# Optimization experiments

Measured on AMD Instinct MI355X. Metric: run time of the kernel, lower is better.

## Reference

```python
import jax, jax.numpy as jnp
import numpy as np

B, N, C = 32, 4096, 768
H = 12
HD = C // H
SCALE = HD ** -0.5


def setup_inputs() -> dict:
    key = jax.random.key(0)
    ks = jax.random.split(key, 5)
    x = jax.random.normal(ks[0], (B, N, C), dtype=jnp.float32)
    s = 1.0 / np.sqrt(C)
    Wq = jax.random.normal(ks[1], (C, C), dtype=jnp.float32) * s
    Wk = jax.random.normal(ks[2], (C, C), dtype=jnp.float32) * s
    Wv = jax.random.normal(ks[3], (C, C), dtype=jnp.float32) * s
    Wp = jax.random.normal(ks[4], (C, C), dtype=jnp.float32) * s
    bp = jnp.zeros((C,), dtype=jnp.float32)
    return {"x": x, "Wq": Wq, "Wk": Wk, "Wv": Wv, "Wp": Wp, "bp": bp}


def reference(x, Wq, Wk, Wv, Wp, bp):
    # single-query (CLS token) cross-attention over N keys
    q = (x[:, 0, :] @ Wq).reshape(B, H, HD)            # [B,H,hd]
    k = (x @ Wk).reshape(B, N, H, HD)                  # [B,N,H,hd]
    v = (x @ Wv).reshape(B, N, H, HD)                  # [B,N,H,hd]
    attn = jnp.einsum('bhd,bnhd->bhn', q, k) * SCALE   # [B,H,N]
    attn = jax.nn.softmax(attn, axis=-1)
    o = jnp.einsum('bhn,bnhd->bhd', attn, v)           # [B,H,hd]
    o = o.reshape(B, 1, C)
    out = o @ Wp + bp                                  # [B,1,C]
    return out
```

## Files before the change

### kernel.cpp

```cpp
#include <hip/hip_runtime.h>
#include <hip/hip_bf16.h>

#define B 32
#define N 4096
#define C 768
#define H 12
#define HD 64

__global__ __launch_bounds__(256) void k1_q(const float* __restrict__ x,
                                            const float* __restrict__ Wq,
                                            float* __restrict__ q) {
    __shared__ float xs[C];
    int b = blockIdx.x / 3;
    int coBase = (blockIdx.x % 3) * 256;
    int t = threadIdx.x;
    for (int i = t; i < C; i += 256) xs[i] = x[(size_t)b * N * C + i];
    __syncthreads();
    int co = coBase + t;
    float acc = 0.f;
    for (int c = 0; c < C; ++c) acc = fmaf(xs[c], Wq[(size_t)c * C + co], acc);
    q[b * C + co] = acc;
}

__global__ __launch_bounds__(256) void k2_qk(const float* __restrict__ q,
                                             const float* __restrict__ Wk,
                                             float* __restrict__ qk,
                                             float* __restrict__ xa) {
    int id = blockIdx.x * 256 + threadIdx.x;
    xa[id] = 0.f;
    int b = id / (H * C);
    int r = id % (H * C);
    int h = r / C;
    int c = r % C;
    const float* wrow = Wk + (size_t)c * C + h * HD;
    const float* qrow = q + b * C + h * HD;
    float acc = 0.f;
#pragma unroll
    for (int j = 0; j < HD / 4; ++j) {
        float4 wv = *(const float4*)(wrow + j * 4);
        float4 qv = *(const float4*)(qrow + j * 4);
        acc += wv.x * qv.x + wv.y * qv.y + wv.z * qv.z + wv.w * qv.w;
    }
    qk[id] = acc * 0.125f;
}

__global__ __launch_bounds__(256) void k3_scores(const float* __restrict__ x,
                                                 const float* __restrict__ qk,
                                                 float* __restrict__ p) {
    __shared__ float4 qks[H * C / 4];
    int b = blockIdx.x >> 5;
    int chunk = blockIdx.x & 31;
    int t = threadIdx.x;
    const float4* qg = (const float4*)(qk + (size_t)b * H * C);
    for (int i = t; i < H * C / 4; i += 256) qks[i] = qg[i];
    __syncthreads();
    int wave = t >> 6, lane = t & 63;
    for (int rr = 0; rr < 32; ++rr) {
        int n = chunk * 128 + wave * 32 + rr;
        const float4* xr = (const float4*)(x + ((size_t)b * N + n) * C);
        float4 X0 = xr[lane];
        float4 X1 = xr[64 + lane];
        float4 X2 = xr[128 + lane];
        float partial[H];
#pragma unroll
        for (int h = 0; h < H; ++h) {
            float4 a0 = qks[h * 192 + lane];
            float4 a1 = qks[h * 192 + 64 + lane];
            float4 a2 = qks[h * 192 + 128 + lane];
            float s = X0.x * a0.x;
            s = fmaf(X0.y, a0.y, s); s = fmaf(X0.z, a0.z, s); s = fmaf(X0.w, a0.w, s);
            s = fmaf(X1.x, a1.x, s); s = fmaf(X1.y, a1.y, s);
            s = fmaf(X1.z, a1.z, s); s = fmaf(X1.w, a1.w, s);
            s = fmaf(X2.x, a2.x, s); s = fmaf(X2.y, a2.y, s);
            s = fmaf(X2.z, a2.z, s); s = fmaf(X2.w, a2.w, s);
            partial[h] = s;
        }
#pragma unroll
        for (int h = 0; h < H; ++h) {
            float v = partial[h];
            for (int off = 32; off > 0; off >>= 1) v += __shfl_xor(v, off);
            partial[h] = v;
        }
        float ov = 0.f;
#pragma unroll
        for (int h = 0; h < H; ++h)
            if (lane == h) ov = partial[h];
        if (lane < H) p[((size_t)b * N + n) * H + lane] = ov;
    }
}

__global__ __launch_bounds__(256) void k4_softmax(float* __restrict__ p) {
    int b = blockIdx.x / H, h = blockIdx.x % H;
    float* pr = p + (size_t)b * N * H + h;
    int t = threadIdx.x;
    float vals[16];
    float m = -1e30f;
#pragma unroll
    for (int i = 0; i < 16; ++i) {
        vals[i] = pr[(size_t)(t + i * 256) * H];
        m = fmaxf(m, vals[i]);
    }
    __shared__ float red[4];
    __shared__ float red2[4];
    for (int off = 32; off > 0; off >>= 1) m = fmaxf(m, __shfl_xor(m, off));
    if ((t & 63) == 0) red[t >> 6] = m;
    __syncthreads();
    m = fmaxf(fmaxf(red[0], red[1]), fmaxf(red[2], red[3]));
    float s = 0.f;
#pragma unroll
    for (int i = 0; i < 16; ++i) {
        vals[i] = __expf(vals[i] - m);
        s += vals[i];
    }
    for (int off = 32; off > 0; off >>= 1) s += __shfl_xor(s, off);
    if ((t & 63) == 0) red2[t >> 6] = s;
    __syncthreads();
    s = red2[0] + red2[1] + red2[2] + red2[3];
    float inv = 1.f / s;
#pragma unroll
    for (int i = 0; i < 16; ++i) pr[(size_t)(t + i * 256) * H] = vals[i] * inv;
}

__global__ __launch_bounds__(256) void k5_xa(const float* __restrict__ x,
                                             const float* __restrict__ p,
                                             float* __restrict__ xa) {
    int gid = blockIdx.x;
    int b = gid / 24;
    int rem = gid % 24;
    int cc = rem / 4;
    int ns = rem % 4;
    int t = threadIdx.x;
    int g = t >> 6;
    int c = cc * 128 + (t & 63) * 2;
    float2 a0 = {0.f, 0.f}, a1 = {0.f, 0.f}, a2 = {0.f, 0.f};
    int n0 = ns * 1024;
    for (int n = n0; n < n0 + 1024; ++n) {
        const float2 xv = *(const float2*)(x + ((size_t)b * N + n) * C + c);
        const float* pr = p + ((size_t)b * N + n) * H + g * 3;
        float p0 = pr[0], p1 = pr[1], p2 = pr[2];
        a0.x = fmaf(p0, xv.x, a0.x); a0.y = fmaf(p0, xv.y, a0.y);
        a1.x = fmaf(p1, xv.x, a1.x); a1.y = fmaf(p1, xv.y, a1.y);
        a2.x = fmaf(p2, xv.x, a2.x); a2.y = fmaf(p2, xv.y, a2.y);
    }
    int h0 = g * 3;
    atomicAdd(&xa[((size_t)b * H + h0    ) * C + c    ], a0.x);
    atomicAdd(&xa[((size_t)b * H + h0    ) * C + c + 1], a0.y);
    atomicAdd(&xa[((size_t)b * H + h0 + 1) * C + c    ], a1.x);
    atomicAdd(&xa[((size_t)b * H + h0 + 1) * C + c + 1], a1.y);
    atomicAdd(&xa[((size_t)b * H + h0 + 2) * C + c    ], a2.x);
    atomicAdd(&xa[((size_t)b * H + h0 + 2) * C + c + 1], a2.y);
}

__global__ __launch_bounds__(256) void k6_o(const float* __restrict__ xa,
                                            const float* __restrict__ Wv,
                                            float* __restrict__ o) {
    int id = blockIdx.x * 256 + threadIdx.x;
    int b = id / C;
    int r = id % C;
    int h = r / HD;
    const float* xr = xa + ((size_t)b * H + h) * C;
    const float* wcol = Wv + r;
    float acc = 0.f;
    for (int c = 0; c < C; ++c) acc = fmaf(xr[c], wcol[(size_t)c * C], acc);
    o[id] = acc;
}

__global__ __launch_bounds__(256) void k7_out(const float* __restrict__ o,
                                              const float* __restrict__ Wp,
                                              const float* __restrict__ bp,
                                              float* __restrict__ out) {
    int id = blockIdx.x * 256 + threadIdx.x;
    int b = id / C;
    int co = id % C;
    const float* orow = o + (size_t)b * C;
    float acc = bp[co];
    for (int c = 0; c < C; ++c) acc = fmaf(orow[c], Wp[(size_t)c * C + co], acc);
    out[id] = acc;
}

extern "C" void kernel_launch(void* const* d_in, const int* in_sizes, int n_in,
                              void* d_out, int out_size, void* d_ws, size_t ws_size,
                              hipStream_t stream) {
    const float* x  = (const float*)d_in[0];
    const float* Wq = (const float*)d_in[1];
    const float* Wk = (const float*)d_in[2];
    const float* Wv = (const float*)d_in[3];
    const float* Wp = (const float*)d_in[4];
    const float* bp = (const float*)d_in[5];
    float* out = (float*)d_out;

    float* ws = (float*)d_ws;
    float* q  = ws;
    float* qk = q + B * C;
    float* p  = qk + (size_t)B * H * C;
    float* xa = p + (size_t)B * N * H;
    float* o  = xa + (size_t)B * H * C;

    k1_q      <<<96,   256, 0, stream>>>(x, Wq, q);
    k2_qk     <<<1152, 256, 0, stream>>>(q, Wk, qk, xa);
    k3_scores <<<1024, 256, 0, stream>>>(x, qk, p);
    k4_softmax<<<384,  256, 0, stream>>>(p);
    k5_xa     <<<768,  256, 0, stream>>>(x, p, xa);
    k6_o      <<<96,   256, 0, stream>>>(xa, Wv, o);
    k7_out    <<<96,   256, 0, stream>>>(o, Wp, bp, out);
}
```

Before: 985.8 us.

## Transpose scores layout, transpose Wk, and restructure score and weighted-sum kernels

Adds a transpose kernel so k2 reads Wk transposed with coalesced row access, and changes the score buffer to [B,H,N] so softmax reads contiguous float4 rows. k3 now uses 512-thread blocks that process two rows at a time with register prefetch of the next rows. k5 is reorganized to stage probabilities in shared memory and keep 12 head accumulators per thread, with a rolling prefetch of x. The aim is to cut strided memory access and the repeated reads of x in the weighted-sum pass. The cost is an extra transpose kernel, more workspace, and higher register pressure in k3 and k5.

```diff
diff --git a/kernel.cpp b/kernel.cpp
--- a/kernel.cpp
+++ b/kernel.cpp
@@ -6,6 +6,19 @@
 #define C 768
 #define H 12
 #define HD 64
+
+__global__ __launch_bounds__(256) void kT(const float* __restrict__ A, float* __restrict__ AT) {
+    __shared__ float tile[32][33];
+    int bx = blockIdx.x % 24, by = blockIdx.x / 24;
+    int tx = threadIdx.x & 31, ty = threadIdx.x >> 5;
+#pragma unroll
+    for (int i = 0; i < 32; i += 8)
+        tile[ty + i][tx] = A[(size_t)(by * 32 + ty + i) * C + bx * 32 + tx];
+    __syncthreads();
+#pragma unroll
+    for (int i = 0; i < 32; i += 8)
+        AT[(size_t)(bx * 32 + ty + i) * C + by * 32 + tx] = tile[tx][ty + i];
+}
 
 __global__ __launch_bounds__(256) void k1_q(const float* __restrict__ x,
                                             const float* __restrict__ Wq,
@@ -23,132 +36,176 @@
 }
 
 __global__ __launch_bounds__(256) void k2_qk(const float* __restrict__ q,
-                                             const float* __restrict__ Wk,
+                                             const float* __restrict__ WkT,
                                              float* __restrict__ qk,
                                              float* __restrict__ xa) {
-    int id = blockIdx.x * 256 + threadIdx.x;
-    xa[id] = 0.f;
-    int b = id / (H * C);
-    int r = id % (H * C);
-    int h = r / C;
-    int c = r % C;
-    const float* wrow = Wk + (size_t)c * C + h * HD;
-    const float* qrow = q + b * C + h * HD;
-    float acc = 0.f;
-#pragma unroll
-    for (int j = 0; j < HD / 4; ++j) {
-        float4 wv = *(const float4*)(wrow + j * 4);
-        float4 qv = *(const float4*)(qrow + j * 4);
-        acc += wv.x * qv.x + wv.y * qv.y + wv.z * qv.z + wv.w * qv.w;
-    }
-    qk[id] = acc * 0.125f;
-}
-
-__global__ __launch_bounds__(256) void k3_scores(const float* __restrict__ x,
+    int b = blockIdx.x / H, h = blockIdx.x % H;
+    int t = threadIdx.x;
+    __shared__ float qs[HD];
+    if (t < HD) qs[t] = q[b * C + h * HD + t];
+    float* xab = xa + ((size_t)b * H + h) * C;
+    xab[t] = 0.f; xab[t + 256] = 0.f; xab[t + 512] = 0.f;
+    __syncthreads();
+    float a0 = 0.f, a1 = 0.f, a2 = 0.f;
+    const float* wbase = WkT + (size_t)h * HD * C;
+    for (int d = 0; d < HD; ++d) {
+        float qd = qs[d];
+        const float* wr = wbase + (size_t)d * C;
+        a0 = fmaf(qd, wr[t], a0);
+        a1 = fmaf(qd, wr[t + 256], a1);
+        a2 = fmaf(qd, wr[t + 512], a2);
+    }
+    float* qkb = qk + ((size_t)b * H + h) * C;
+    qkb[t] = a0 * 0.125f; qkb[t + 256] = a1 * 0.125f; qkb[t + 512] = a2 * 0.125f;
+}
+
+__global__ __launch_bounds__(512) void k3_scores(const float* __restrict__ x,
                                                  const float* __restrict__ qk,
-                                                 float* __restrict__ p) {
-    __shared__ float4 qks[H * C / 4];
+                                                 float* __restrict__ p2) {
+    __shared__ float4 qks[H * 192];
     int b = blockIdx.x >> 5;
     int chunk = blockIdx.x & 31;
     int t = threadIdx.x;
     const float4* qg = (const float4*)(qk + (size_t)b * H * C);
-    for (int i = t; i < H * C / 4; i += 256) qks[i] = qg[i];
+    for (int i = t; i < H * 192; i += 512) qks[i] = qg[i];
     __syncthreads();
     int wave = t >> 6, lane = t & 63;
-    for (int rr = 0; rr < 32; ++rr) {
-        int n = chunk * 128 + wave * 32 + rr;
-        const float4* xr = (const float4*)(x + ((size_t)b * N + n) * C);
-        float4 X0 = xr[lane];
-        float4 X1 = xr[64 + lane];
-        float4 X2 = xr[128 + lane];
-        float partial[H];
+    int n0 = chunk * 128 + wave * 16;
+    const float4* xbase = (const float4*)(x + (size_t)b * N * C);
+    float4 Xc[2][3], Xn[2][3];
+#pragma unroll
+    for (int r = 0; r < 2; ++r)
+#pragma unroll
+        for (int j = 0; j < 3; ++j)
+            Xc[r][j] = xbase[(size_t)(n0 + r) * 192 + j * 64 + lane];
+    for (int pr = 0; pr < 8; ++pr) {
+        int n = n0 + pr * 2;
+        if (pr < 7) {
+#pragma unroll
+            for (int r = 0; r < 2; ++r)
+#pragma unroll
+                for (int j = 0; j < 3; ++j)
+                    Xn[r][j] = xbase[(size_t)(n + 2 + r) * 192 + j * 64 + lane];
+        }
+        float s0[H], s1[H];
 #pragma unroll
         for (int h = 0; h < H; ++h) {
             float4 a0 = qks[h * 192 + lane];
             float4 a1 = qks[h * 192 + 64 + lane];
             float4 a2 = qks[h * 192 + 128 + lane];
-            float s = X0.x * a0.x;
-            s = fmaf(X0.y, a0.y, s); s = fmaf(X0.z, a0.z, s); s = fmaf(X0.w, a0.w, s);
-            s = fmaf(X1.x, a1.x, s); s = fmaf(X1.y, a1.y, s);
-            s = fmaf(X1.z, a1.z, s); s = fmaf(X1.w, a1.w, s);
-            s = fmaf(X2.x, a2.x, s); s = fmaf(X2.y, a2.y, s);
-            s = fmaf(X2.z, a2.z, s); s = fmaf(X2.w, a2.w, s);
-            partial[h] = s;
+            float u = Xc[0][0].x * a0.x;
+            u = fmaf(Xc[0][0].y, a0.y, u); u = fmaf(Xc[0][0].z, a0.z, u); u = fmaf(Xc[0][0].w, a0.w, u);
+            u = fmaf(Xc[0][1].x, a1.x, u); u = fmaf(Xc[0][1].y, a1.y, u);
+            u = fmaf(Xc[0][1].z, a1.z, u); u = fmaf(Xc[0][1].w, a1.w, u);
+            u = fmaf(Xc[0][2].x, a2.x, u); u = fmaf(Xc[0][2].y, a2.y, u);
+            u = fmaf(Xc[0][2].z, a2.z, u); u = fmaf(Xc[0][2].w, a2.w, u);
+            s0[h] = u;
+            float v = Xc[1][0].x * a0.x;
+            v = fmaf(Xc[1][0].y, a0.y, v); v = fmaf(Xc[1][0].z, a0.z, v); v = fmaf(Xc[1][0].w, a0.w, v);
+            v = fmaf(Xc[1][1].x, a1.x, v); v = fmaf(Xc[1][1].y, a1.y, v);
+            v = fmaf(Xc[1][1].z, a1.z, v); v = fmaf(Xc[1][1].w, a1.w, v);
+            v = fmaf(Xc[1][2].x, a2.x, v); v = fmaf(Xc[1][2].y, a2.y, v);
+            v = fmaf(Xc[1][2].z, a2.z, v); v = fmaf(Xc[1][2].w, a2.w, v);
+            s1[h] = v;
         }
 #pragma unroll
         for (int h = 0; h < H; ++h) {
-            float v = partial[h];
-            for (int off = 32; off > 0; off >>= 1) v += __shfl_xor(v, off);
-            partial[h] = v;
-        }
-        float ov = 0.f;
+            float u = s0[h], v = s1[h];
+            for (int off = 32; off; off >>= 1) {
+                u += __shfl_xor(u, off);
+                v += __shfl_xor(v, off);
+            }
+            s0[h] = u; s1[h] = v;
+        }
+        float o0 = 0.f, o1 = 0.f;
 #pragma unroll
         for (int h = 0; h < H; ++h)
-            if (lane == h) ov = partial[h];
-        if (lane < H) p[((size_t)b * N + n) * H + lane] = ov;
-    }
-}
-
-__global__ __launch_bounds__(256) void k4_softmax(float* __restrict__ p) {
-    int b = blockIdx.x / H, h = blockIdx.x % H;
-    float* pr = p + (size_t)b * N * H + h;
-    int t = threadIdx.x;
-    float vals[16];
+            if (lane == h) { o0 = s0[h]; o1 = s1[h]; }
+        if (lane < H) {
+            p2[((size_t)b * H + lane) * N + n]     = o0;
+            p2[((size_t)b * H + lane) * N + n + 1] = o1;
+        }
+#pragma unroll
+        for (int r = 0; r < 2; ++r)
+#pragma unroll
+            for (int j = 0; j < 3; ++j)
+                Xc[r][j] = Xn[r][j];
+    }
+}
+
+__global__ __launch_bounds__(256) void k4_softmax(float* __restrict__ p2) {
+    int t = threadIdx.x;
+    float4* pr = (float4*)(p2 + (size_t)blockIdx.x * N);
+    float4 v[4];
     float m = -1e30f;
 #pragma unroll
-    for (int i = 0; i < 16; ++i) {
-        vals[i] = pr[(size_t)(t + i * 256) * H];
-        m = fmaxf(m, vals[i]);
-    }
-    __shared__ float red[4];
-    __shared__ float red2[4];
-    for (int off = 32; off > 0; off >>= 1) m = fmaxf(m, __shfl_xor(m, off));
+    for (int i = 0; i < 4; ++i) {
+        v[i] = pr[t + i * 256];
+        m = fmaxf(m, fmaxf(fmaxf(v[i].x, v[i].y), fmaxf(v[i].z, v[i].w)));
+    }
+    __shared__ float red[4], red2[4];
+    for (int off = 32; off; off >>= 1) m = fmaxf(m, __shfl_xor(m, off));
     if ((t & 63) == 0) red[t >> 6] = m;
     __syncthreads();
     m = fmaxf(fmaxf(red[0], red[1]), fmaxf(red[2], red[3]));
     float s = 0.f;
 #pragma unroll
-    for (int i = 0; i < 16; ++i) {
-        vals[i] = __expf(vals[i] - m);
-        s += vals[i];
-    }
-    for (int off = 32; off > 0; off >>= 1) s += __shfl_xor(s, off);
+    for (int i = 0; i < 4; ++i) {
+        v[i].x = __expf(v[i].x - m); v[i].y = __expf(v[i].y - m);
+        v[i].z = __expf(v[i].z - m); v[i].w = __expf(v[i].w - m);
+        s += v[i].x + v[i].y + v[i].z + v[i].w;
+    }
+    for (int off = 32; off; off >>= 1) s += __shfl_xor(s, off);
     if ((t & 63) == 0) red2[t >> 6] = s;
     __syncthreads();
     s = red2[0] + red2[1] + red2[2] + red2[3];
     float inv = 1.f / s;
 #pragma unroll
-    for (int i = 0; i < 16; ++i) pr[(size_t)(t + i * 256) * H] = vals[i] * inv;
-}
-
-__global__ __launch_bounds__(256) void k5_xa(const float* __restrict__ x,
-                                             const float* __restrict__ p,
+    for (int i = 0; i < 4; ++i) {
+        v[i].x *= inv; v[i].y *= inv; v[i].z *= inv; v[i].w *= inv;
+        pr[t + i * 256] = v[i];
+    }
+}
+
+__global__ __launch_bounds__(192) void k5_xa(const float* __restrict__ x,
+                                             const float* __restrict__ p2,
                                              float* __restrict__ xa) {
-    int gid = blockIdx.x;
-    int b = gid / 24;
-    int rem = gid % 24;
-    int cc = rem / 4;
-    int ns = rem % 4;
-    int t = threadIdx.x;
-    int g = t >> 6;
-    int c = cc * 128 + (t & 63) * 2;
-    float2 a0 = {0.f, 0.f}, a1 = {0.f, 0.f}, a2 = {0.f, 0.f};
-    int n0 = ns * 1024;
-    for (int n = n0; n < n0 + 1024; ++n) {
-        const float2 xv = *(const float2*)(x + ((size_t)b * N + n) * C + c);
-        const float* pr = p + ((size_t)b * N + n) * H + g * 3;
-        float p0 = pr[0], p1 = pr[1], p2 = pr[2];
-        a0.x = fmaf(p0, xv.x, a0.x); a0.y = fmaf(p0, xv.y, a0.y);
-        a1.x = fmaf(p1, xv.x, a1.x); a1.y = fmaf(p1, xv.y, a1.y);
-        a2.x = fmaf(p2, xv.x, a2.x); a2.y = fmaf(p2, xv.y, a2.y);
-    }
-    int h0 = g * 3;
-    atomicAdd(&xa[((size_t)b * H + h0    ) * C + c    ], a0.x);
-    atomicAdd(&xa[((size_t)b * H + h0    ) * C + c + 1], a0.y);
-    atomicAdd(&xa[((size_t)b * H + h0 + 1) * C + c    ], a1.x);
-    atomicAdd(&xa[((size_t)b * H + h0 + 1) * C + c + 1], a1.y);
-    atomicAdd(&xa[((size_t)b * H + h0 + 2) * C + c    ], a2.x);
-    atomicAdd(&xa[((size_t)b * H + h0 + 2) * C + c + 1], a2.y);
+    __shared__ float ps[H][128];
+    int b = blockIdx.x >> 5, ns = blockIdx.x & 31;
+    int n0 = ns * 128;
+    int t = threadIdx.x;
+    for (int i = t; i < H * 128; i += 192) {
+        int h = i >> 7, j = i & 127;
+        ps[h][j] = p2[((size_t)b * H + h) * N + n0 + j];
+    }
+    __syncthreads();
+    const float4* xr = (const float4*)(x + ((size_t)b * N + n0) * C);
+    float4 acc[H];
+#pragma unroll
+    for (int h = 0; h < H; ++h) acc[h] = make_float4(0.f, 0.f, 0.f, 0.f);
+    float4 x0 = xr[t], x1 = xr[192 + t], x2 = xr[384 + t];
+    for (int r = 0; r < 128; ++r) {
+        float4 cur = x0;
+        x0 = x1; x1 = x2;
+        int rn = (r + 3 < 128) ? (r + 3) : r;
+        x2 = xr[rn * 192 + t];
+#pragma unroll
+        for (int h = 0; h < H; ++h) {
+            float pv = ps[h][r];
+            acc[h].x = fmaf(pv, cur.x, acc[h].x);
+            acc[h].y = fmaf(pv, cur.y, acc[h].y);
+            acc[h].z = fmaf(pv, cur.z, acc[h].z);
+            acc[h].w = fmaf(pv, cur.w, acc[h].w);
+        }
+    }
+#pragma unroll
+    for (int h = 0; h < H; ++h) {
+        float* dst = xa + ((size_t)b * H + h) * C + 4 * t;
+        atomicAdd(dst + 0, acc[h].x);
+        atomicAdd(dst + 1, acc[h].y);
+        atomicAdd(dst + 2, acc[h].z);
+        atomicAdd(dst + 3, acc[h].w);
+    }
 }
 
 __global__ __launch_bounds__(256) void k6_o(const float* __restrict__ xa,
@@ -189,18 +246,20 @@
     const float* bp = (const float*)d_in[5];
     float* out = (float*)d_out;
 
-    float* ws = (float*)d_ws;
-    float* q  = ws;
-    float* qk = q + B * C;
-    float* p  = qk + (size_t)B * H * C;
-    float* xa = p + (size_t)B * N * H;
-    float* o  = xa + (size_t)B * H * C;
-
+    float* ws  = (float*)d_ws;
+    float* q   = ws;
+    float* qk  = q + B * C;
+    float* p2  = qk + (size_t)B * H * C;
+    float* xa  = p2 + (size_t)B * H * N;
+    float* o   = xa + (size_t)B * H * C;
+    float* WkT = o + B * C;
+
+    kT        <<<576,  256, 0, stream>>>(Wk, WkT);
     k1_q      <<<96,   256, 0, stream>>>(x, Wq, q);
-    k2_qk     <<<1152, 256, 0, stream>>>(q, Wk, qk, xa);
-    k3_scores <<<1024, 256, 0, stream>>>(x, qk, p);
-    k4_softmax<<<384,  256, 0, stream>>>(p);
-    k5_xa     <<<768,  256, 0, stream>>>(x, p, xa);
+    k2_qk     <<<384,  256, 0, stream>>>(q, WkT, qk, xa);
+    k3_scores <<<1024, 512, 0, stream>>>(x, qk, p2);
+    k4_softmax<<<384,  256, 0, stream>>>(p2);
+    k5_xa     <<<1024, 192, 0, stream>>>(x, p2, xa);
     k6_o      <<<96,   256, 0, stream>>>(xa, Wv, o);
     k7_out    <<<96,   256, 0, stream>>>(o, Wp, bp, out);
 }
```

New measurement: 1.320 ms. +33.9%, slower.
